# Kernel tuning notes

Hardware: AMD Instinct MI355X
Metric: run time of the kernel (lower is better)

## Reference

```python
import jax, jax.numpy as jnp
import numpy as np

H, HID = 2, 64
N_USER, N_POST, N_ENT = 50000, 100000, 20000
EDGES = [("publish", 100000, N_USER, N_POST), ("repost", 200000, N_USER, N_POST), ("contain", 200000, N_POST, N_ENT), ("interact", 400000, N_USER, N_USER), ("follow", 400000, N_USER, N_USER), ("similar", 250000, N_POST, N_POST)]


def setup_inputs() -> dict:
    key = jax.random.key(0)
    ks = iter(jax.random.split(key, 64))
    d = {}
    d["x_post"] = jax.random.normal(next(ks), (N_POST, 768), jnp.float32)
    d["x_user"] = jax.random.normal(next(ks), (N_USER, 32), jnp.float32)
    d["x_entity"] = jax.random.normal(next(ks), (N_ENT, 64), jnp.float32)
    for name, E, ns, nd in EDGES:
        d["src_" + name] = jax.random.randint(next(ks), (E,), 0, ns, jnp.int32)
        d["dst_" + name] = jax.random.randint(next(ks), (E,), 0, nd, jnp.int32)
    def lin(k, o, i):
        return jax.random.normal(k, (o, i), jnp.float32) / np.sqrt(i)
    d["post_proj_w"] = lin(next(ks), HID, 768); d["post_proj_b"] = jnp.zeros((HID,), jnp.float32)
    d["user_proj_w"] = lin(next(ks), HID, 32); d["user_proj_b"] = jnp.zeros((HID,), jnp.float32)
    d["ent_proj_w"] = lin(next(ks), HID, 64); d["ent_proj_b"] = jnp.zeros((HID,), jnp.float32)
    # 2 layers x 6 relations of bipartite GATConv params, stacked
    d["W_src"] = jax.random.normal(next(ks), (2, 6, H * HID, HID), jnp.float32) / np.sqrt(HID)
    d["W_dst"] = jax.random.normal(next(ks), (2, 6, H * HID, HID), jnp.float32) / np.sqrt(HID)
    d["a_src"] = jax.random.normal(next(ks), (2, 6, H, HID), jnp.float32) * 0.1
    d["a_dst"] = jax.random.normal(next(ks), (2, 6, H, HID), jnp.float32) * 0.1
    d["gat_b"] = jnp.zeros((2, 6, HID), jnp.float32)
    d["cls_w1"] = lin(next(ks), HID // 2, HID); d["cls_b1"] = jnp.zeros((HID // 2,), jnp.float32)
    d["cls_w2"] = lin(next(ks), 1, HID // 2); d["cls_b2"] = jnp.zeros((1,), jnp.float32)
    return d


def _gat(x_src, x_dst, src, dst, w_s, w_d, a_s, a_d, b):
    """PyG GATConv, bipartite, heads=H, concat=False, no self loops."""
    n_dst = x_dst.shape[0]
    hs = (x_src @ w_s.T).reshape(-1, H, HID)   # [N_src, H, C]
    hd = (x_dst @ w_d.T).reshape(-1, H, HID)   # [N_dst, H, C]
    al_s = jnp.einsum("nhc,hc->nh", hs, a_s)
    al_d = jnp.einsum("nhc,hc->nh", hd, a_d)
    e = jax.nn.leaky_relu(al_s[src] + al_d[dst], negative_slope=0.2)  # [E, H]
    m = jax.ops.segment_max(e, dst, num_segments=n_dst)
    m = jnp.where(jnp.isfinite(m), m, 0.0)  # empty segments -> -inf, unused
    p = jnp.exp(e - m[dst])
    s = jax.ops.segment_sum(p, dst, num_segments=n_dst)
    alpha = p / (s[dst] + 1e-16)
    out = jax.ops.segment_sum(hs[src] * alpha[:, :, None], dst, num_segments=n_dst)
    return out.mean(axis=1) + b  # concat=False -> mean over heads, plus bias


def reference(x_post, x_user, x_entity, src_publish, dst_publish, src_repost, dst_repost, src_contain, dst_contain, src_interact, dst_interact, src_follow, dst_follow, src_similar, dst_similar, post_proj_w, post_proj_b, user_proj_w, user_proj_b, ent_proj_w, ent_proj_b, W_src, W_dst, a_src, a_dst, gat_b, cls_w1, cls_b1, cls_w2, cls_b2):
    h_post = x_post @ post_proj_w.T + post_proj_b
    h_user = x_user @ user_proj_w.T + user_proj_b
    h_ent = x_entity @ ent_proj_w.T + ent_proj_b
    for l in range(2):
        def g(r, xs, xd, s, dd):
            return _gat(xs, xd, s, dd, W_src[l, r], W_dst[l, r], a_src[l, r], a_dst[l, r], gat_b[l, r])
        new_post = (g(0, h_user, h_post, src_publish, dst_publish)
                    + g(1, h_user, h_post, src_repost, dst_repost)
                    + g(5, h_post, h_post, src_similar, dst_similar))
        new_ent = g(2, h_post, h_ent, src_contain, dst_contain)
        new_user = (g(3, h_user, h_user, src_interact, dst_interact)
                    + g(4, h_user, h_user, src_follow, dst_follow))
        h_post, h_user, h_ent = jax.nn.relu(new_post), jax.nn.relu(new_user), jax.nn.relu(new_ent)
    h = jax.nn.relu(h_post @ cls_w1.T + cls_b1)  # dropout is eval-mode identity
    return (h @ cls_w2.T + cls_b2).squeeze(-1)
```

## Files before the change

### kernel.cpp

```cpp
#include <hip/hip_runtime.h>

#define NPOST 100000
#define NUSER 50000
#define NENT  20000
#define NDTOT 420000
#define EACT  1350000
#define NSCANBLK 206
#define NT_AL 150000

typedef short short8 __attribute__((ext_vector_type(8)));
typedef float f32x4 __attribute__((ext_vector_type(4)));
typedef unsigned short ushort4v __attribute__((ext_vector_type(4)));

static __device__ __forceinline__ unsigned short f2bf(float x){
  union { float f; unsigned u; } v; v.f = x;
  unsigned r = v.u + 0x7FFF + ((v.u >> 16) & 1);
  return (unsigned short)(r >> 16);
}
static __device__ __forceinline__ float bf2f(unsigned short h){
  union { unsigned u; float f; } v; v.u = ((unsigned)h) << 16;
  return v.f;
}

struct EdgeMeta {
  const int* src[6];
  const int* dst[6];
  int E[6];
  int degoff[6];
};

struct PrepArgs {
  const float *Wp, *Wu, *We, *Wsrc, *Wdst, *asrc, *adst, *gatb;
  unsigned short *WpH, *WpL, *WuH, *WuL, *WeH, *WeL, *lbH, *lbL;
  float *weff_s, *weff_d, *bsum;
};


__global__ void k_histprep(EdgeMeta em, int* __restrict__ deg, PrepArgs P){
  if (blockIdx.y < 5){
    const int map[5] = {0, 1, 3, 4, 5};
    int r = map[blockIdx.y];
    int e = blockIdx.x * blockDim.x + threadIdx.x;
    if (e >= em.E[r]) return;
    atomicAdd(&deg[em.degoff[r] + em.dst[r][e]], 1);
    return;
  }
  int idx = blockIdx.x * blockDim.x + threadIdx.x;
  if (idx < 49152){
    float x = P.Wp[idx];
    unsigned short h = f2bf(x);
    P.WpH[idx] = h; P.WpL[idx] = f2bf(x - bf2f(h));
  } else if (idx < 51200){
    int i = idx - 49152;
    float x = P.Wu[i];
    unsigned short h = f2bf(x);
    P.WuH[i] = h; P.WuL[i] = f2bf(x - bf2f(h));
  } else if (idx < 55296){
    int i = idx - 51200;
    float x = P.We[i];
    unsigned short h = f2bf(x);
    P.WeH[i] = h; P.WeL[i] = f2bf(x - bf2f(h));
  } else if (idx < 153600){
    int i = idx - 55296;
    const int off[6]  = {0, 24576, 40960, 49152, 73728, 90112};
    const int Ks[6]   = {384, 256, 128, 384, 256, 128};
    int seg = 5;
    #pragma unroll
    for (int s = 4; s >= 0; s--) if (i < off[s + 1]) seg = s;
    int l = seg / 3, type = seg % 3;
    int K = Ks[seg];
    int rem = i - off[seg];
    int n = rem / K, k = rem - n * K;
    int slot = k >> 7, head = (k >> 6) & 1, kk = k & 63;
    int rel;
    if (type == 0)      rel = (slot == 0) ? 0 : (slot == 1 ? 1 : 5);
    else if (type == 1) rel = (slot == 0) ? 3 : 4;
    else                rel = 2;
    int m = l * 6 + rel;
    float x = P.Wsrc[(size_t)m * 8192 + (head * 64 + n) * 64 + kk];
    unsigned short h = f2bf(x);
    P.lbH[i] = h; P.lbL[i] = f2bf(x - bf2f(h));
  } else if (idx < 156672){
    int i = idx - 153600;
    const float* W; const float* a; float* o; int j;
    if (i < 1536){ W = P.Wsrc; a = P.asrc; o = P.weff_s; j = i; }
    else         { W = P.Wdst; a = P.adst; o = P.weff_d; j = i - 1536; }
    int m = j >> 7;
    int rem = j & 127;
    int hh = rem >> 6, k = rem & 63;
    const float* Wm = W + (size_t)m * 8192;
    const float* am = a + (size_t)m * 128;
    float acc = 0.f;
    #pragma unroll 8
    for (int c = 0; c < 64; c++)
      acc += Wm[(hh * 64 + c) * 64 + k] * am[hh * 64 + c];
    o[j] = acc;
  } else if (idx < 157056){
    int i = idx - 156672;
    int c = i & 63;
    int lt = i >> 6;
    int l = lt / 3, t = lt % 3;
    float v;
    if (t == 0)      v = P.gatb[(l*6+0)*64+c] + P.gatb[(l*6+1)*64+c] + P.gatb[(l*6+5)*64+c];
    else if (t == 1) v = P.gatb[(l*6+3)*64+c] + P.gatb[(l*6+4)*64+c];
    else             v = P.gatb[(l*6+2)*64+c];
    P.bsum[lt * 64 + c] = v;
  }
}


__global__ __launch_bounds__(256) void k_scanA(const int* __restrict__ deg,
                                               int* __restrict__ rowstart,
                                               int* __restrict__ blocksum){
  __shared__ int sums[256];
  int t = threadIdx.x;
  int base = blockIdx.x * 2048 + t * 8;
  int v[8]; int s = 0;
  #pragma unroll
  for (int i = 0; i < 8; i++){
    int j = base + i;
    v[i] = (j < NDTOT) ? deg[j] : 0;
    s += v[i];
  }
  sums[t] = s;
  __syncthreads();
  for (int off = 1; off < 256; off <<= 1){
    int x = (t >= off) ? sums[t - off] : 0;
    __syncthreads();
    sums[t] += x;
    __syncthreads();
  }
  int excl = (t > 0) ? sums[t - 1] : 0;
  if (t == 255) blocksum[blockIdx.x] = sums[255];
  int run = excl;
  #pragma unroll
  for (int i = 0; i < 8; i++){
    int j = base + i;
    if (j < NDTOT) rowstart[j] = run;
    run += v[i];
  }
}

__global__ __launch_bounds__(256) void k_scanC(const int* __restrict__ blocksum,
                                               int* __restrict__ rowstart,
                                               int* __restrict__ cursor){
  __shared__ int s[256];
  int t = threadIdx.x;
  int k = blockIdx.x >> 3;
  s[t] = (t < k) ? blocksum[t] : 0;
  __syncthreads();
  for (int off = 128; off > 0; off >>= 1){
    if (t < off) s[t] += s[t + off];
    __syncthreads();
  }
  int pre = s[0];
  int j = blockIdx.x * 256 + t;
  if (j < NDTOT){
    int v = rowstart[j] + pre;
    rowstart[j] = v;
    cursor[j] = v;
  }
  if (j == 0) rowstart[NDTOT] = EACT;
}

__global__ void k_scatter(EdgeMeta em, int* __restrict__ cursor,
                          int* __restrict__ csr_src, int* __restrict__ csr_row){
  const int map[5] = {0, 1, 3, 4, 5};
  int r = map[blockIdx.y];
  int e = blockIdx.x * blockDim.x + threadIdx.x;
  if (e >= em.E[r]) return;
  int d = em.dst[r][e];
  int w = em.degoff[r] + d;
  int pos = atomicAdd(&cursor[w], 1);
  csr_src[pos] = em.src[r][e];
  csr_row[pos] = w;
}


struct AlArgs {
  const float *h0, *h1;
  const float *ws, *wd;
  float *als, *ald;
  int layer;
};

static __device__ __forceinline__ float2 dot2w(const float4* hr, const float* __restrict__ w){
  const float4* w0 = (const float4*)w;
  const float4* w1 = (const float4*)(w + 64);
  float a0 = 0.f, a1 = 0.f;
  #pragma unroll
  for (int q = 0; q < 16; q++){
    float4 v = hr[q];
    float4 x0 = w0[q], x1 = w1[q];
    a0 += v.x*x0.x + v.y*x0.y + v.z*x0.z + v.w*x0.w;
    a1 += v.x*x1.x + v.y*x1.y + v.z*x1.z + v.w*x1.w;
  }
  return make_float2(a0, a1);
}

__global__ __launch_bounds__(256) void k_al_all(AlArgs A){
  int i = blockIdx.x * blockDim.x + threadIdx.x;
  if (i >= NT_AL) return;
  float4 hr[16];
  if (i < NPOST){
    int n = i;
    const float4* hp = (const float4*)(A.h0 + (size_t)n * 64);
    #pragma unroll
    for (int q = 0; q < 16; q++) hr[q] = hp[q];
    *(float2*)(A.als + (size_t)(300000 + n) * 2) = dot2w(hr, A.ws + 5 * 128);
    *(float2*)(A.ald + (size_t)(0      + n) * 2) = dot2w(hr, A.wd + 0 * 128);
    *(float2*)(A.ald + (size_t)(100000 + n) * 2) = dot2w(hr, A.wd + 1 * 128);
    *(float2*)(A.ald + (size_t)(320000 + n) * 2) = dot2w(hr, A.wd + 5 * 128);
  } else {
    int n = i - NPOST;
    const float4* hp = (const float4*)(A.h1 + (size_t)n * 64);
    #pragma unroll
    for (int q = 0; q < 16; q++) hr[q] = hp[q];
    *(float2*)(A.als + (size_t)(0      + n) * 2) = dot2w(hr, A.ws + 0 * 128);
    *(float2*)(A.als + (size_t)(50000  + n) * 2) = dot2w(hr, A.ws + 1 * 128);
    if (A.layer == 0){
      *(float2*)(A.als + (size_t)(200000 + n) * 2) = dot2w(hr, A.ws + 3 * 128);
      *(float2*)(A.als + (size_t)(250000 + n) * 2) = dot2w(hr, A.ws + 4 * 128);
      *(float2*)(A.ald + (size_t)(220000 + n) * 2) = dot2w(hr, A.wd + 3 * 128);
      *(float2*)(A.ald + (size_t)(270000 + n) * 2) = dot2w(hr, A.wd + 4 * 128);
    }
  }
}


struct EdgepArgs {
  const int *csr_src, *csr_row;
  const float *als, *ald;
  float2 *pcsr;
  int thr, off, nE;
};

__global__ __launch_bounds__(256) void k_edgep(EdgepArgs A){
  int e0 = blockIdx.x * blockDim.x + threadIdx.x;
  if (e0 >= A.nE) return;
  int e = e0 < A.thr ? e0 : e0 + A.off;
  int w = A.csr_row[e];
  int soffr;
  if      (w < 100000) soffr = 0;
  else if (w < 200000) soffr = 50000;
  else if (w < 270000) soffr = 200000;
  else if (w < 320000) soffr = 250000;
  else                 soffr = 300000;
  int sidx = A.csr_src[e];
  float2 as = *(const float2*)(A.als + (size_t)(soffr + sidx) * 2);
  float2 ad = *(const float2*)(A.ald + (size_t)w * 2);
  float e0v = as.x + ad.x, e1v = as.y + ad.y;
  e0v = e0v > 0.f ? e0v : 0.2f * e0v;
  e1v = e1v > 0.f ? e1v : 0.2f * e1v;
  A.pcsr[e] = make_float2(__expf(e0v), __expf(e1v));
}


static __device__ __forceinline__ int aswz(int row, int k){
  return row * 128 + ((((k >> 3) ^ (row & 7))) << 3) + (k & 7);
}

static __device__ __forceinline__ void agg_row(const int* __restrict__ csr_src,
                                               const float2* __restrict__ pcsr,
                                               const float* __restrict__ h, int l16,
                                               int rs, int re,
                                               f32x4& a0, f32x4& a1, float& s0, float& s1){
  int e = rs;
  for (; e + 3 < re; e += 4){
    int sa = csr_src[e];
    int sb = csr_src[e + 1];
    int sc = csr_src[e + 2];
    int sd = csr_src[e + 3];
    float2 pa = pcsr[e];
    float2 pb = pcsr[e + 1];
    float2 pc = pcsr[e + 2];
    float2 pd = pcsr[e + 3];
    f32x4 ha = *(const f32x4*)(h + (size_t)sa * 64 + l16 * 4);
    f32x4 hb = *(const f32x4*)(h + (size_t)sb * 64 + l16 * 4);
    f32x4 hc = *(const f32x4*)(h + (size_t)sc * 64 + l16 * 4);
    f32x4 hd = *(const f32x4*)(h + (size_t)sd * 64 + l16 * 4);
    #pragma unroll
    for (int j = 0; j < 4; j++){ a0[j] = fmaf(pa.x, ha[j], a0[j]); a1[j] = fmaf(pa.y, ha[j], a1[j]); }
    s0 += pa.x; s1 += pa.y;
    #pragma unroll
    for (int j = 0; j < 4; j++){ a0[j] = fmaf(pb.x, hb[j], a0[j]); a1[j] = fmaf(pb.y, hb[j], a1[j]); }
    s0 += pb.x; s1 += pb.y;
    #pragma unroll
    for (int j = 0; j < 4; j++){ a0[j] = fmaf(pc.x, hc[j], a0[j]); a1[j] = fmaf(pc.y, hc[j], a1[j]); }
    s0 += pc.x; s1 += pc.y;
    #pragma unroll
    for (int j = 0; j < 4; j++){ a0[j] = fmaf(pd.x, hd[j], a0[j]); a1[j] = fmaf(pd.y, hd[j], a1[j]); }
    s0 += pd.x; s1 += pd.y;
  }
  for (; e + 1 < re; e += 2){
    int sa = csr_src[e];
    int sb = csr_src[e + 1];
    float2 pa = pcsr[e];
    float2 pb = pcsr[e + 1];
    f32x4 ha = *(const f32x4*)(h + (size_t)sa * 64 + l16 * 4);
    f32x4 hb = *(const f32x4*)(h + (size_t)sb * 64 + l16 * 4);
    #pragma unroll
    for (int j = 0; j < 4; j++){ a0[j] = fmaf(pa.x, ha[j], a0[j]); a1[j] = fmaf(pa.y, ha[j], a1[j]); }
    s0 += pa.x; s1 += pa.y;
    #pragma unroll
    for (int j = 0; j < 4; j++){ a0[j] = fmaf(pb.x, hb[j], a0[j]); a1[j] = fmaf(pb.y, hb[j], a1[j]); }
    s0 += pb.x; s1 += pb.y;
  }
  if (e < re){
    int sa = csr_src[e];
    float2 pa = pcsr[e];
    f32x4 ha = *(const f32x4*)(h + (size_t)sa * 64 + l16 * 4);
    #pragma unroll
    for (int j = 0; j < 4; j++){ a0[j] = fmaf(pa.x, ha[j], a0[j]); a1[j] = fmaf(pa.y, ha[j], a1[j]); }
    s0 += pa.x; s1 += pa.y;
  }
}

struct FJob {
  const unsigned short *BH, *BL;
  const float *bias;
  float *C;
  int N, nslots, K;
  int wb0, wb1, wb2;
  int ss0, ss1, ss2;
};
struct FArgs {
  const int *rowstart, *csr_src;
  const float2 *pcsr;
  const float *h0, *h1;
  FJob j0, j1;
  int nb0;
  const float *cw1, *cb1, *cw2, *cb2;
  float *out;
};

template<int CLS>
__global__ __launch_bounds__(256) void k_fused(FArgs A){
  __shared__ __align__(16) unsigned short sbuf[2 * 64 * 128];
  unsigned short* sAh = sbuf;
  unsigned short* sAl = sbuf + 64 * 128;
  int b = blockIdx.x;
  FJob J = (b < A.nb0) ? A.j0 : A.j1;
  int boff = (b < A.nb0) ? 0 : A.nb0;
  int r0 = (b - boff) * 64;
  int t = threadIdx.x;
  int w = t >> 6, lane = t & 63;
  int q = lane >> 4, m15 = lane & 15;
  int g2 = t >> 4, l16 = t & 15;
  int wr = w & 1, wc = w >> 1;
  f32x4 acc[2][2];
  #pragma unroll
  for (int i = 0; i < 2; i++)
    #pragma unroll
    for (int j = 0; j < 2; j++)
      acc[i][j] = (f32x4){0.f, 0.f, 0.f, 0.f};

  for (int s = 0; s < J.nslots; s++){
    int wbase = (s == 0) ? J.wb0 : ((s == 1) ? J.wb1 : J.wb2);
    int ssel  = (s == 0) ? J.ss0 : ((s == 1) ? J.ss1 : J.ss2);
    const float* h = ssel ? A.h1 : A.h0;
    for (int rr = g2; rr < 64; rr += 16){
      int grow = r0 + rr;
      int rs = 0, re = 0;
      if (grow < J.N){
        int wg = wbase + grow;
        rs = A.rowstart[wg];
        re = A.rowstart[wg + 1];
      }
      f32x4 a0 = (f32x4){0.f,0.f,0.f,0.f};
      f32x4 a1 = (f32x4){0.f,0.f,0.f,0.f};
      float s0 = 0.f, s1 = 0.f;
      agg_row(A.csr_src, A.pcsr, h, l16, rs, re, a0, a1, s0, s1);
      float r0v = s0 > 0.f ? 0.5f / s0 : 0.f;
      float r1v = s1 > 0.f ? 0.5f / s1 : 0.f;
      ushort4v H0, H1, L0, L1;
      #pragma unroll
      for (int j = 0; j < 4; j++){
        float v0 = a0[j] * r0v;
        float v1 = a1[j] * r1v;
        unsigned short h0v = f2bf(v0); H0[j] = h0v; L0[j] = f2bf(v0 - bf2f(h0v));
        unsigned short h1v = f2bf(v1); H1[j] = h1v; L1[j] = f2bf(v1 - bf2f(h1v));
      }
      *(ushort4v*)(sAh + aswz(rr, l16 * 4))      = H0;
      *(ushort4v*)(sAh + aswz(rr, 64 + l16 * 4)) = H1;
      *(ushort4v*)(sAl + aswz(rr, l16 * 4))      = L0;
      *(ushort4v*)(sAl + aswz(rr, 64 + l16 * 4)) = L1;
    }
    __syncthreads();
    #pragma unroll
    for (int kc = 0; kc < 4; kc++){
      int gk = s * 128 + kc * 32;
      short8 ah[2], al_[2];
      #pragma unroll
      for (int i = 0; i < 2; i++){
        int mrow = wr * 32 + i * 16 + m15;
        ah[i]  = *(const short8*)(sAh + aswz(mrow, kc * 32 + q * 8));
        al_[i] = *(const short8*)(sAl + aswz(mrow, kc * 32 + q * 8));
      }
      #pragma unroll
      for (int j = 0; j < 2; j++){
        int bn = wc * 32 + j * 16 + m15;
        short8 bh = *(const short8*)(J.BH + (size_t)bn * J.K + gk + q * 8);
        short8 bl = *(const short8*)(J.BL + (size_t)bn * J.K + gk + q * 8);
        #pragma unroll
        for (int i = 0; i < 2; i++){
          acc[i][j] = __builtin_amdgcn_mfma_f32_16x16x32_bf16(ah[i],  bh, acc[i][j], 0, 0, 0);
          acc[i][j] = __builtin_amdgcn_mfma_f32_16x16x32_bf16(ah[i],  bl, acc[i][j], 0, 0, 0);
          acc[i][j] = __builtin_amdgcn_mfma_f32_16x16x32_bf16(al_[i], bh, acc[i][j], 0, 0, 0);
        }
      }
    }
    __syncthreads();
  }
  if (!CLS){
    #pragma unroll
    for (int j = 0; j < 2; j++){
      int col = wc * 32 + j * 16 + m15;
      float bv = J.bias[col];
      #pragma unroll
      for (int i = 0; i < 2; i++){
        #pragma unroll
        for (int r = 0; r < 4; r++){
          int row = r0 + wr * 32 + i * 16 + q * 4 + r;
          if (row < J.N){
            float vv = acc[i][j][r] + bv;
            J.C[(size_t)row * 64 + col] = vv > 0.f ? vv : 0.f;
          }
        }
      }
    }
  } else {
    float* ht  = (float*)sbuf;
    float* w1s = ht + 64 * 68;
    float* b1s = w1s + 2048;
    float* w2s = b1s + 32;
    #pragma unroll
    for (int j = 0; j < 2; j++){
      int col = wc * 32 + j * 16 + m15;
      float bv = J.bias[col];
      #pragma unroll
      for (int i = 0; i < 2; i++){
        #pragma unroll
        for (int r = 0; r < 4; r++){
          int lrow = wr * 32 + i * 16 + q * 4 + r;
          float vv = acc[i][j][r] + bv;
          ht[lrow * 68 + col] = vv > 0.f ? vv : 0.f;
        }
      }
    }
    for (int i = t; i < 2048; i += 256) w1s[i] = A.cw1[i];
    if (t < 32){ b1s[t] = A.cb1[t]; w2s[t] = A.cw2[t]; }
    __syncthreads();
    if (t < 64){
      int row = r0 + t;
      if (row < J.N){
        float4 hr[16];
        const float4* hp = (const float4*)(ht + t * 68);
        #pragma unroll
        for (int q16 = 0; q16 < 16; q16++) hr[q16] = hp[q16];
        float o = A.cb2[0];
        #pragma unroll 4
        for (int j = 0; j < 32; j++){
          float dacc = b1s[j];
          const float4* wr_ = (const float4*)(w1s + j * 64);
          #pragma unroll
          for (int q16 = 0; q16 < 16; q16++){
            float4 wv = wr_[q16]; float4 v = hr[q16];
            dacc += wv.x*v.x + wv.y*v.y + wv.z*v.z + wv.w*v.w;
          }
          dacc = dacc > 0.f ? dacc : 0.f;
          o += w2s[j] * dacc;
        }
        A.out[row] = o;
      }
    }
  }
}


static __device__ __forceinline__ int swz(int row, int k){
  return row * 32 + ((((k >> 3) ^ ((row >> 2) & 3))) << 3) + (k & 7);
}

struct GemmJob {
  const float* A32;
  const unsigned short* AH; const unsigned short* AL;
  const unsigned short* BH; const unsigned short* BL;
  const float* bias; float* C;
  int N; int K;
};
struct GemmJobs { GemmJob j0, j1, j2; int nb0, nb1; };

template<int ASRC, int RELU>
__global__ __launch_bounds__(256) void k_mfgemm3(GemmJobs G){
  __shared__ __align__(16) unsigned short sAh[128 * 32];
  __shared__ __align__(16) unsigned short sAl[128 * 32];
  __shared__ __align__(16) unsigned short sBh[64 * 32];
  __shared__ __align__(16) unsigned short sBl[64 * 32];
  int b = blockIdx.x;
  GemmJob jb = G.j0;
  int boff = 0;
  if (b >= G.nb1){ jb = G.j2; boff = G.nb1; }
  else if (b >= G.nb0){ jb = G.j1; boff = G.nb0; }
  const float* A32 = jb.A32;
  const unsigned short* AH = jb.AH;
  const unsigned short* AL = jb.AL;
  const unsigned short* BH = jb.BH;
  const unsigned short* BL = jb.BL;
  int N = jb.N, K = jb.K;

  int t = threadIdx.x;
  int w = t >> 6, lane = t & 63;
  int q = lane >> 4, m15 = lane & 15;
  int r0 = (b - boff) * 128;
  f32x4 acc[2][4];
  #pragma unroll
  for (int i = 0; i < 2; i++)
    #pragma unroll
    for (int j = 0; j < 4; j++)
      acc[i][j] = (f32x4){0.f, 0.f, 0.f, 0.f};

  int arow = t >> 1, akb = (t & 1) * 16;
  int brow = t >> 2, bkb = (t & 3) * 8;

  for (int k0 = 0; k0 < K; k0 += 32){
    int gr = r0 + arow;
    if (ASRC == 0){
      float v[16];
      if (gr < N){
        const float4* ap = (const float4*)(A32 + (size_t)gr * K + k0 + akb);
        #pragma unroll
        for (int i = 0; i < 4; i++){
          float4 f = ap[i];
          v[i*4+0] = f.x; v[i*4+1] = f.y; v[i*4+2] = f.z; v[i*4+3] = f.w;
        }
      } else {
        #pragma unroll
        for (int i = 0; i < 16; i++) v[i] = 0.f;
      }
      short8 h0, h1, l0, l1;
      #pragma unroll
      for (int i = 0; i < 8; i++){
        unsigned short hh = f2bf(v[i]);
        h0[i] = (short)hh; l0[i] = (short)f2bf(v[i] - bf2f(hh));
        unsigned short hj = f2bf(v[8+i]);
        h1[i] = (short)hj; l1[i] = (short)f2bf(v[8+i] - bf2f(hj));
      }
      *(short8*)(sAh + swz(arow, akb))     = h0;
      *(short8*)(sAh + swz(arow, akb + 8)) = h1;
      *(short8*)(sAl + swz(arow, akb))     = l0;
      *(short8*)(sAl + swz(arow, akb + 8)) = l1;
    } else {
      short8 h0 = {0,0,0,0,0,0,0,0}, h1 = {0,0,0,0,0,0,0,0};
      short8 l0 = {0,0,0,0,0,0,0,0}, l1 = {0,0,0,0,0,0,0,0};
      if (gr < N){
        const short8* hp = (const short8*)(AH + (size_t)gr * K + k0 + akb);
        const short8* lp = (const short8*)(AL + (size_t)gr * K + k0 + akb);
        h0 = hp[0]; h1 = hp[1];
        l0 = lp[0]; l1 = lp[1];
      }
      *(short8*)(sAh + swz(arow, akb))     = h0;
      *(short8*)(sAh + swz(arow, akb + 8)) = h1;
      *(short8*)(sAl + swz(arow, akb))     = l0;
      *(short8*)(sAl + swz(arow, akb + 8)) = l1;
    }
    {
      short8 bh = *(const short8*)(BH + (size_t)brow * K + k0 + bkb);
      short8 bl = *(const short8*)(BL + (size_t)brow * K + k0 + bkb);
      *(short8*)(sBh + swz(brow, bkb)) = bh;
      *(short8*)(sBl + swz(brow, bkb)) = bl;
    }
    __syncthreads();
    short8 ah[2], al_[2];
    #pragma unroll
    for (int i = 0; i < 2; i++){
      int mrow = w * 32 + i * 16 + m15;
      ah[i]  = *(const short8*)(sAh + swz(mrow, q * 8));
      al_[i] = *(const short8*)(sAl + swz(mrow, q * 8));
    }
    #pragma unroll
    for (int j = 0; j < 4; j++){
      int bn = j * 16 + m15;
      short8 bh = *(const short8*)(sBh + swz(bn, q * 8));
      short8 bl = *(const short8*)(sBl + swz(bn, q * 8));
      #pragma unroll
      for (int i = 0; i < 2; i++){
        acc[i][j] = __builtin_amdgcn_mfma_f32_16x16x32_bf16(ah[i],  bh, acc[i][j], 0, 0, 0);
        acc[i][j] = __builtin_amdgcn_mfma_f32_16x16x32_bf16(ah[i],  bl, acc[i][j], 0, 0, 0);
        acc[i][j] = __builtin_amdgcn_mfma_f32_16x16x32_bf16(al_[i], bh, acc[i][j], 0, 0, 0);
      }
    }
    __syncthreads();
  }
  const float* bias = jb.bias;
  float* C = jb.C;
  #pragma unroll
  for (int j = 0; j < 4; j++){
    int col = j * 16 + m15;
    float bv = bias[col];
    #pragma unroll
    for (int i = 0; i < 2; i++){
      #pragma unroll
      for (int r = 0; r < 4; r++){
        int row = r0 + w * 32 + i * 16 + q * 4 + r;
        if (row < N){
          float vv = acc[i][j][r] + bv;
          if (RELU) vv = vv > 0.f ? vv : 0.f;
          C[(size_t)row * 64 + col] = vv;
        }
      }
    }
  }
}


static inline size_t align256(size_t x){ return (x + 255) & ~(size_t)255; }

extern "C" void kernel_launch(void* const* d_in, const int* in_sizes, int n_in,
                              void* d_out, int out_size, void* d_ws, size_t ws_size,
                              hipStream_t stream){
  (void)in_sizes; (void)n_in; (void)out_size; (void)ws_size;
  const float* x_post = (const float*)d_in[0];
  const float* x_user = (const float*)d_in[1];
  EdgeMeta em;
  for (int r = 0; r < 6; r++){
    em.src[r] = (const int*)d_in[3 + 2*r];
    em.dst[r] = (const int*)d_in[4 + 2*r];
  }
  const int Earr[6] = {100000, 200000, 200000, 400000, 400000, 250000};
  const int dgo[6]  = {0, 100000, 200000, 220000, 270000, 320000};
  for (int r = 0; r < 6; r++){ em.E[r] = Earr[r]; em.degoff[r] = dgo[r]; }

  const float* Wp   = (const float*)d_in[15]; const float* bp = (const float*)d_in[16];
  const float* Wu   = (const float*)d_in[17]; const float* bu = (const float*)d_in[18];
  const float* We   = (const float*)d_in[19];
  const float* Wsrc = (const float*)d_in[21];
  const float* Wdst = (const float*)d_in[22];
  const float* asrc = (const float*)d_in[23];
  const float* adst = (const float*)d_in[24];
  const float* gatb = (const float*)d_in[25];
  const float* cw1  = (const float*)d_in[26]; const float* cb1 = (const float*)d_in[27];
  const float* cw2  = (const float*)d_in[28]; const float* cb2 = (const float*)d_in[29];
  float* out = (float*)d_out;

  const int NN[2] = {NPOST, NUSER};

  char* p = (char*)d_ws;
  auto alloc = [&](size_t bytes){ char* r = p; p += align256(bytes); return r; };
  float* hA[2]; float* hB[2];
  for (int i = 0; i < 2; i++) hA[i] = (float*)alloc((size_t)NN[i] * 64 * 4);
  for (int i = 0; i < 2; i++) hB[i] = (float*)alloc((size_t)NN[i] * 64 * 4);
  float* als = (float*)alloc((size_t)400000 * 2 * 4);
  float* ald = (float*)alloc((size_t)NDTOT * 2 * 4);
  float* weff_s = (float*)alloc(1536 * 4);
  float* weff_d = (float*)alloc(1536 * 4);
  unsigned short* WpH = (unsigned short*)alloc(768 * 64 * 2);
  unsigned short* WpL = (unsigned short*)alloc(768 * 64 * 2);
  unsigned short* WuH = (unsigned short*)alloc(32 * 64 * 2);
  unsigned short* WuL = (unsigned short*)alloc(32 * 64 * 2);
  unsigned short* WeH = (unsigned short*)alloc(64 * 64 * 2);
  unsigned short* WeL = (unsigned short*)alloc(64 * 64 * 2);
  unsigned short* lbH = (unsigned short*)alloc(98304 * 2);
  unsigned short* lbL = (unsigned short*)alloc(98304 * 2);
  float* bsum   = (float*)alloc(6 * 64 * 4);
  int* deg      = (int*)alloc((size_t)NDTOT * 4);
  int* rowstart = (int*)alloc((size_t)(NDTOT + 1) * 4);
  int* cursor   = (int*)alloc((size_t)NDTOT * 4);
  int* csr_src  = (int*)alloc((size_t)EACT * 4);
  int* csr_row  = (int*)alloc((size_t)EACT * 4);
  float2* pcsr  = (float2*)alloc((size_t)EACT * 8);
  int* blocksum = (int*)alloc((size_t)NSCANBLK * 4);

  hipMemsetAsync(deg, 0, (size_t)NDTOT * 4, stream);
  PrepArgs P = {Wp, Wu, We, Wsrc, Wdst, asrc, adst, gatb,
                WpH, WpL, WuH, WuL, WeH, WeL, lbH, lbL,
                weff_s, weff_d, bsum};
  k_histprep<<<dim3(1563, 6), 256, 0, stream>>>(em, deg, P);
  k_scanA<<<NSCANBLK, 256, 0, stream>>>(deg, rowstart, blocksum);
  k_scanC<<<(NDTOT + 255) / 256, 256, 0, stream>>>(blocksum, rowstart, cursor);
  k_scatter<<<dim3(1563, 5), 256, 0, stream>>>(em, cursor, csr_src, csr_row);

  GemmJobs GP;
  GP.j0 = {x_post, nullptr, nullptr, WpH, WpL, bp, hA[0], NPOST, 768};
  GP.j1 = {x_user, nullptr, nullptr, WuH, WuL, bu, hA[1], NUSER, 32};
  GP.j2 = GP.j1;
  GP.nb0 = 782; GP.nb1 = 1173;
  k_mfgemm3<0, 0><<<1173, 256, 0, stream>>>(GP);

  const int segoff[6] = {0, 24576, 40960, 49152, 73728, 90112};

  float* cur[2] = {hA[0], hA[1]};
  float* nxt[2] = {hB[0], hB[1]};

  for (int l = 0; l < 2; l++){
    AlArgs AA = {cur[0], cur[1], weff_s + l * 768, weff_d + l * 768, als, ald, l};
    k_al_all<<<(NT_AL + 255) / 256, 256, 0, stream>>>(AA);

    int nE  = (l == 0) ? EACT : 550000;
    int thr = (l == 0) ? EACT : 300000;
    int off = (l == 0) ? 0 : 800000;
    EdgepArgs EP = {csr_src, csr_row, als, ald, pcsr, thr, off, nE};
    k_edgep<<<(nE + 255) / 256, 256, 0, stream>>>(EP);

    FArgs FA;
    FA.rowstart = rowstart; FA.csr_src = csr_src; FA.pcsr = pcsr;
    FA.h0 = cur[0]; FA.h1 = cur[1];
    FA.cw1 = cw1; FA.cb1 = cb1; FA.cw2 = cw2; FA.cb2 = cb2; FA.out = out;
    FA.j0 = {lbH + segoff[l*3+0], lbL + segoff[l*3+0], bsum + (l*3+0) * 64, nxt[0],
             NPOST, 3, 384, 0, 100000, 320000, 1, 1, 0};
    if (l == 0){
      FA.j1 = {lbH + segoff[l*3+1], lbL + segoff[l*3+1], bsum + (l*3+1) * 64, nxt[1],
               NUSER, 2, 256, 220000, 270000, 0, 1, 1, 0};
      FA.nb0 = 1563;
      k_fused<0><<<1563 + 782, 256, 0, stream>>>(FA);
    } else {
      FA.j1 = FA.j0;
      FA.nb0 = 1563;
      k_fused<1><<<1563, 256, 0, stream>>>(FA);
    }
    for (int i = 0; i < 2; i++){ float* tmp = cur[i]; cur[i] = nxt[i]; nxt[i] = tmp; }
  }
}
```

Measured before the change: 573.7 us.

## Fuse attention-logit computation into projection and aggregation kernel epilogues

Removes the separate k_al_all kernel, which re-read every node feature row to compute per-relation attention logits. The projection GEMM and the layer-0 fused aggregation kernel now stage each output tile in shared memory and compute the logit dot products for the next stage in their epilogue. This saves two launches and a full pass over node features, at the cost of extra syncs, shared-memory staging, and epilogue work done by only 64 threads per block. The obsolete bf16-input GEMM path is also dropped.

After: 678.9 us. 18.3% more time.

```diff
diff --git a/kernel.cpp b/kernel.cpp
--- a/kernel.cpp
+++ b/kernel.cpp
@@ -6,7 +6,6 @@
 #define NDTOT 420000
 #define EACT  1350000
 #define NSCANBLK 206
-#define NT_AL 150000
 
 typedef short short8 __attribute__((ext_vector_type(8)));
 typedef float f32x4 __attribute__((ext_vector_type(4)));
@@ -177,13 +176,6 @@
 }
 
 
-struct AlArgs {
-  const float *h0, *h1;
-  const float *ws, *wd;
-  float *als, *ald;
-  int layer;
-};
-
 static __device__ __forceinline__ float2 dot2w(const float4* hr, const float* __restrict__ w){
   const float4* w0 = (const float4*)w;
   const float4* w1 = (const float4*)(w + 64);
@@ -196,35 +188,6 @@
     a1 += v.x*x1.x + v.y*x1.y + v.z*x1.z + v.w*x1.w;
   }
   return make_float2(a0, a1);
-}
-
-__global__ __launch_bounds__(256) void k_al_all(AlArgs A){
-  int i = blockIdx.x * blockDim.x + threadIdx.x;
-  if (i >= NT_AL) return;
-  float4 hr[16];
-  if (i < NPOST){
-    int n = i;
-    const float4* hp = (const float4*)(A.h0 + (size_t)n * 64);
-    #pragma unroll
-    for (int q = 0; q < 16; q++) hr[q] = hp[q];
-    *(float2*)(A.als + (size_t)(300000 + n) * 2) = dot2w(hr, A.ws + 5 * 128);
-    *(float2*)(A.ald + (size_t)(0      + n) * 2) = dot2w(hr, A.wd + 0 * 128);
-    *(float2*)(A.ald + (size_t)(100000 + n) * 2) = dot2w(hr, A.wd + 1 * 128);
-    *(float2*)(A.ald + (size_t)(320000 + n) * 2) = dot2w(hr, A.wd + 5 * 128);
-  } else {
-    int n = i - NPOST;
-    const float4* hp = (const float4*)(A.h1 + (size_t)n * 64);
-    #pragma unroll
-    for (int q = 0; q < 16; q++) hr[q] = hp[q];
-    *(float2*)(A.als + (size_t)(0      + n) * 2) = dot2w(hr, A.ws + 0 * 128);
-    *(float2*)(A.als + (size_t)(50000  + n) * 2) = dot2w(hr, A.ws + 1 * 128);
-    if (A.layer == 0){
-      *(float2*)(A.als + (size_t)(200000 + n) * 2) = dot2w(hr, A.ws + 3 * 128);
-      *(float2*)(A.als + (size_t)(250000 + n) * 2) = dot2w(hr, A.ws + 4 * 128);
-      *(float2*)(A.ald + (size_t)(220000 + n) * 2) = dot2w(hr, A.wd + 3 * 128);
-      *(float2*)(A.ald + (size_t)(270000 + n) * 2) = dot2w(hr, A.wd + 4 * 128);
-    }
-  }
 }
 
 
@@ -323,6 +286,9 @@
   int N, nslots, K;
   int wb0, wb1, wb2;
   int ss0, ss1, ss2;
+  int nal;
+  const float* alw[4];
+  float* aldst[4];
 };
 struct FArgs {
   const int *rowstart, *csr_src;
@@ -425,6 +391,38 @@
           if (row < J.N){
             float vv = acc[i][j][r] + bv;
             J.C[(size_t)row * 64 + col] = vv > 0.f ? vv : 0.f;
+          }
+        }
+      }
+    }
+    if (J.nal > 0){
+      float* ht = (float*)sbuf;
+      __syncthreads();
+      #pragma unroll
+      for (int j = 0; j < 2; j++){
+        int col = wc * 32 + j * 16 + m15;
+        float bv = J.bias[col];
+        #pragma unroll
+        for (int i = 0; i < 2; i++){
+          #pragma unroll
+          for (int r = 0; r < 4; r++){
+            int lrow = wr * 32 + i * 16 + q * 4 + r;
+            float vv = acc[i][j][r] + bv;
+            ht[lrow * 68 + col] = vv > 0.f ? vv : 0.f;
+          }
+        }
+      }
+      __syncthreads();
+      if (t < 64){
+        int row = r0 + t;
+        if (row < J.N){
+          float4 hr[16];
+          const float4* hp = (const float4*)(ht + t * 68);
+          #pragma unroll
+          for (int q16 = 0; q16 < 16; q16++) hr[q16] = hp[q16];
+          for (int k2 = 0; k2 < J.nal; k2++){
+            float2 d = dot2w(hr, J.alw[k2]);
+            *(float2*)(J.aldst[k2] + (size_t)row * 2) = d;
           }
         }
       }
@@ -484,27 +482,25 @@
 
 struct GemmJob {
   const float* A32;
-  const unsigned short* AH; const unsigned short* AL;
   const unsigned short* BH; const unsigned short* BL;
   const float* bias; float* C;
   int N; int K;
+  int nal;
+  const float* alw[6];
+  float* aldst[6];
 };
-struct GemmJobs { GemmJob j0, j1, j2; int nb0, nb1; };
-
-template<int ASRC, int RELU>
-__global__ __launch_bounds__(256) void k_mfgemm3(GemmJobs G){
-  __shared__ __align__(16) unsigned short sAh[128 * 32];
-  __shared__ __align__(16) unsigned short sAl[128 * 32];
-  __shared__ __align__(16) unsigned short sBh[64 * 32];
-  __shared__ __align__(16) unsigned short sBl[64 * 32];
+struct GemmJobs { GemmJob j0, j1; int nb0; };
+
+__global__ __launch_bounds__(256) void k_proj(GemmJobs G){
+  __shared__ __align__(16) unsigned short smem[12288];
+  unsigned short* sAh = smem;
+  unsigned short* sAl = smem + 4096;
+  unsigned short* sBh = smem + 8192;
+  unsigned short* sBl = smem + 10240;
   int b = blockIdx.x;
-  GemmJob jb = G.j0;
-  int boff = 0;
-  if (b >= G.nb1){ jb = G.j2; boff = G.nb1; }
-  else if (b >= G.nb0){ jb = G.j1; boff = G.nb0; }
+  GemmJob jb = (b < G.nb0) ? G.j0 : G.j1;
+  int boff = (b < G.nb0) ? 0 : G.nb0;
   const float* A32 = jb.A32;
-  const unsigned short* AH = jb.AH;
-  const unsigned short* AL = jb.AL;
   const unsigned short* BH = jb.BH;
   const unsigned short* BL = jb.BL;
   int N = jb.N, K = jb.K;
@@ -525,45 +521,30 @@
 
   for (int k0 = 0; k0 < K; k0 += 32){
     int gr = r0 + arow;
-    if (ASRC == 0){
-      float v[16];
-      if (gr < N){
-        const float4* ap = (const float4*)(A32 + (size_t)gr * K + k0 + akb);
-        #pragma unroll
-        for (int i = 0; i < 4; i++){
-          float4 f = ap[i];
-          v[i*4+0] = f.x; v[i*4+1] = f.y; v[i*4+2] = f.z; v[i*4+3] = f.w;
-        }
-      } else {
-        #pragma unroll
-        for (int i = 0; i < 16; i++) v[i] = 0.f;
-      }
-      short8 h0, h1, l0, l1;
-      #pragma unroll
-      for (int i = 0; i < 8; i++){
-        unsigned short hh = f2bf(v[i]);
-        h0[i] = (short)hh; l0[i] = (short)f2bf(v[i] - bf2f(hh));
-        unsigned short hj = f2bf(v[8+i]);
-        h1[i] = (short)hj; l1[i] = (short)f2bf(v[8+i] - bf2f(hj));
-      }
-      *(short8*)(sAh + swz(arow, akb))     = h0;
-      *(short8*)(sAh + swz(arow, akb + 8)) = h1;
-      *(short8*)(sAl + swz(arow, akb))     = l0;
-      *(short8*)(sAl + swz(arow, akb + 8)) = l1;
+    float v[16];
+    if (gr < N){
+      const float4* ap = (const float4*)(A32 + (size_t)gr * K + k0 + akb);
+      #pragma unroll
+      for (int i = 0; i < 4; i++){
+        float4 f = ap[i];
+        v[i*4+0] = f.x; v[i*4+1] = f.y; v[i*4+2] = f.z; v[i*4+3] = f.w;
+      }
     } else {
-      short8 h0 = {0,0,0,0,0,0,0,0}, h1 = {0,0,0,0,0,0,0,0};
-      short8 l0 = {0,0,0,0,0,0,0,0}, l1 = {0,0,0,0,0,0,0,0};
-      if (gr < N){
-        const short8* hp = (const short8*)(AH + (size_t)gr * K + k0 + akb);
-        const short8* lp = (const short8*)(AL + (size_t)gr * K + k0 + akb);
-        h0 = hp[0]; h1 = hp[1];
-        l0 = lp[0]; l1 = lp[1];
-      }
-      *(short8*)(sAh + swz(arow, akb))     = h0;
-      *(short8*)(sAh + swz(arow, akb + 8)) = h1;
-      *(short8*)(sAl + swz(arow, akb))     = l0;
-      *(short8*)(sAl + swz(arow, akb + 8)) = l1;
-    }
+      #pragma unroll
+      for (int i = 0; i < 16; i++) v[i] = 0.f;
+    }
+    short8 h0, h1, l0, l1;
+    #pragma unroll
+    for (int i = 0; i < 8; i++){
+      unsigned short hh = f2bf(v[i]);
+      h0[i] = (short)hh; l0[i] = (short)f2bf(v[i] - bf2f(hh));
+      unsigned short hj = f2bf(v[8+i]);
+      h1[i] = (short)hj; l1[i] = (short)f2bf(v[8+i] - bf2f(hj));
+    }
+    *(short8*)(sAh + swz(arow, akb))     = h0;
+    *(short8*)(sAh + swz(arow, akb + 8)) = h1;
+    *(short8*)(sAl + swz(arow, akb))     = l0;
+    *(short8*)(sAl + swz(arow, akb + 8)) = l1;
     {
       short8 bh = *(const short8*)(BH + (size_t)brow * K + k0 + bkb);
       short8 bl = *(const short8*)(BL + (size_t)brow * K + k0 + bkb);
@@ -604,9 +585,40 @@
       for (int r = 0; r < 4; r++){
         int row = r0 + w * 32 + i * 16 + q * 4 + r;
         if (row < N){
-          float vv = acc[i][j][r] + bv;
-          if (RELU) vv = vv > 0.f ? vv : 0.f;
-          C[(size_t)row * 64 + col] = vv;
+          C[(size_t)row * 64 + col] = acc[i][j][r] + bv;
+        }
+      }
+    }
+  }
+  float* ht = (float*)smem;
+  for (int half = 0; half < 2; half++){
+    __syncthreads();
+    if ((w >> 1) == half){
+      #pragma unroll
+      for (int j = 0; j < 4; j++){
+        int col = j * 16 + m15;
+        float bv = bias[col];
+        #pragma unroll
+        for (int i = 0; i < 2; i++){
+          #pragma unroll
+          for (int r = 0; r < 4; r++){
+            int lrow = (w & 1) * 32 + i * 16 + q * 4 + r;
+            ht[lrow * 68 + col] = acc[i][j][r] + bv;
+          }
+        }
+      }
+    }
+    __syncthreads();
+    if (t < 64){
+      int row = r0 + half * 64 + t;
+      if (row < N){
+        float4 hr[16];
+        const float4* hp = (const float4*)(ht + t * 68);
+        #pragma unroll
+        for (int q16 = 0; q16 < 16; q16++) hr[q16] = hp[q16];
+        for (int k2 = 0; k2 < jb.nal; k2++){
+          float2 d = dot2w(hr, jb.alw[k2]);
+          *(float2*)(jb.aldst[k2] + (size_t)row * 2) = d;
         }
       }
     }
@@ -680,12 +692,20 @@
   k_scanC<<<(NDTOT + 255) / 256, 256, 0, stream>>>(blocksum, rowstart, cursor);
   k_scatter<<<dim3(1563, 5), 256, 0, stream>>>(em, cursor, csr_src, csr_row);
 
+  const float* ws0 = weff_s;       const float* wd0 = weff_d;
+  const float* ws1 = weff_s + 768; const float* wd1 = weff_d + 768;
+
   GemmJobs GP;
-  GP.j0 = {x_post, nullptr, nullptr, WpH, WpL, bp, hA[0], NPOST, 768};
-  GP.j1 = {x_user, nullptr, nullptr, WuH, WuL, bu, hA[1], NUSER, 32};
-  GP.j2 = GP.j1;
-  GP.nb0 = 782; GP.nb1 = 1173;
-  k_mfgemm3<0, 0><<<1173, 256, 0, stream>>>(GP);
+  GP.j0 = {x_post, WpH, WpL, bp, hA[0], NPOST, 768,
+           4,
+           {ws0 + 5*128, wd0 + 0, wd0 + 1*128, wd0 + 5*128, nullptr, nullptr},
+           {als + 600000, ald + 0, ald + 200000, ald + 640000, nullptr, nullptr}};
+  GP.j1 = {x_user, WuH, WuL, bu, hA[1], NUSER, 32,
+           6,
+           {ws0 + 0, ws0 + 1*128, ws0 + 3*128, ws0 + 4*128, wd0 + 3*128, wd0 + 4*128},
+           {als + 0, als + 100000, als + 400000, als + 500000, ald + 440000, ald + 540000}};
+  GP.nb0 = 782;
+  k_proj<<<1173, 256, 0, stream>>>(GP);
 
   const int segoff[6] = {0, 24576, 40960, 49152, 73728, 90112};
 
@@ -693,9 +713,6 @@
   float* nxt[2] = {hB[0], hB[1]};
 
   for (int l = 0; l < 2; l++){
-    AlArgs AA = {cur[0], cur[1], weff_s + l * 768, weff_d + l * 768, als, ald, l};
-    k_al_all<<<(NT_AL + 255) / 256, 256, 0, stream>>>(AA);
-
     int nE  = (l == 0) ? EACT : 550000;
     int thr = (l == 0) ? EACT : 300000;
     int off = (l == 0) ? 0 : 800000;
@@ -706,14 +723,23 @@
     FA.rowstart = rowstart; FA.csr_src = csr_src; FA.pcsr = pcsr;
     FA.h0 = cur[0]; FA.h1 = cur[1];
     FA.cw1 = cw1; FA.cb1 = cb1; FA.cw2 = cw2; FA.cb2 = cb2; FA.out = out;
-    FA.j0 = {lbH + segoff[l*3+0], lbL + segoff[l*3+0], bsum + (l*3+0) * 64, nxt[0],
-             NPOST, 3, 384, 0, 100000, 320000, 1, 1, 0};
     if (l == 0){
-      FA.j1 = {lbH + segoff[l*3+1], lbL + segoff[l*3+1], bsum + (l*3+1) * 64, nxt[1],
-               NUSER, 2, 256, 220000, 270000, 0, 1, 1, 0};
+      FA.j0 = {lbH + segoff[0], lbL + segoff[0], bsum + 0 * 64, nxt[0],
+               NPOST, 3, 384, 0, 100000, 320000, 1, 1, 0,
+               4,
+               {ws1 + 5*128, wd1 + 0, wd1 + 1*128, wd1 + 5*128},
+               {als + 600000, ald + 0, ald + 200000, ald + 640000}};
+      FA.j1 = {lbH + segoff[1], lbL + segoff[1], bsum + 1 * 64, nxt[1],
+               NUSER, 2, 256, 220000, 270000, 0, 1, 1, 0,
+               2,
+               {ws1 + 0, ws1 + 1*128, nullptr, nullptr},
+               {als + 0, als + 100000, nullptr, nullptr}};
       FA.nb0 = 1563;
       k_fused<0><<<1563 + 782, 256, 0, stream>>>(FA);
     } else {
+      FA.j0 = {lbH + segoff[3], lbL + segoff[3], bsum + 3 * 64, nxt[0],
+               NPOST, 3, 384, 0, 100000, 320000, 1, 1, 0,
+               0, {nullptr, nullptr, nullptr, nullptr}, {nullptr, nullptr, nullptr, nullptr}};
       FA.j1 = FA.j0;
       FA.nb0 = 1563;
       k_fused<1><<<1563, 256, 0, stream>>>(FA);
```
